# Kernel tuning notes

Hardware: AMD Instinct MI355X
Metric: run time of the kernel (lower is better)

## Reference

```python
import jax, jax.numpy as jnp
import numpy as np

N = 100000
E = 1600000
D_IN, D_HID, D_OUT = 128, 32, 32
NEG_SLOPE = 0.2
EPS = 1e-16


def setup_inputs() -> dict:
    key = jax.random.key(0)
    ks = jax.random.split(key, 9)
    x = jax.random.normal(ks[0], (N, D_IN), dtype=jnp.float32)
    edge_index = jax.random.randint(ks[1], (2, E), 0, N, dtype=jnp.int64)
    W1 = jax.random.normal(ks[2], (D_IN, D_HID), dtype=jnp.float32) / np.sqrt(D_IN)
    b1 = jnp.zeros((D_HID,), dtype=jnp.float32)
    W2 = jax.random.normal(ks[3], (D_HID, D_OUT), dtype=jnp.float32) / np.sqrt(D_HID)
    att_src = jax.random.normal(ks[4], (D_OUT,), dtype=jnp.float32) / np.sqrt(D_OUT)
    att_dst = jax.random.normal(ks[5], (D_OUT,), dtype=jnp.float32) / np.sqrt(D_OUT)
    b2 = jnp.zeros((D_OUT,), dtype=jnp.float32)
    return {"x": x, "edge_index": edge_index, "W1": W1, "b1": b1,
            "W2": W2, "att_src": att_src, "att_dst": att_dst, "b2": b2}


def _add_self_loops(edge_index, n):
    loop = jnp.arange(n, dtype=edge_index.dtype)
    src = jnp.concatenate([edge_index[0], loop])
    dst = jnp.concatenate([edge_index[1], loop])
    return src, dst


def _gcn_conv(x, src, dst, W, b, n):
    # symmetric normalization with self-loops already included
    deg = jax.ops.segment_sum(jnp.ones_like(dst, dtype=x.dtype), dst, num_segments=n)
    dis = jnp.where(deg > 0, jax.lax.rsqrt(jnp.maximum(deg, 1.0)), 0.0)
    h = x @ W                               # [N, H]
    norm = dis[src] * dis[dst]              # [E2]
    msg = norm[:, None] * h[src]            # [E2, H]
    return jax.ops.segment_sum(msg, dst, num_segments=n) + b


def _gat_conv(x, src, dst, W, att_src, att_dst, b, n):
    g = x @ W                               # [N, H]
    a_s = g @ att_src                       # [N]
    a_d = g @ att_dst                       # [N]
    e = a_s[src] + a_d[dst]                 # [E2]
    e = jnp.where(e > 0, e, NEG_SLOPE * e)  # leaky_relu(0.2)
    # segment softmax over edges grouped by destination node
    emax = jax.ops.segment_max(e, dst, num_segments=n)
    ee = jnp.exp(e - emax[dst])
    esum = jax.ops.segment_sum(ee, dst, num_segments=n)
    alpha = ee / (esum[dst] + EPS)
    msg = alpha[:, None] * g[src]           # [E2, H]
    return jax.ops.segment_sum(msg, dst, num_segments=n) + b


def reference(x, edge_index, W1, b1, W2, att_src, att_dst, b2):
    n = x.shape[0]
    src, dst = _add_self_loops(edge_index, n)
    h = _gcn_conv(x, src, dst, W1, b1, n)
    h = jax.nn.relu(h)
    out = _gat_conv(h, src, dst, W2, att_src, att_dst, b2, n)
    return out
```

## Files before the change

kernel.cpp:

```cpp
#include <hip/hip_runtime.h>
#include <cstdint>
#include <cstddef>

#define D_IN   128
#define D_HID  32
#define D_OUT  32
#define NEG_SLOPE 0.2f
#define EPS_F  1e-16f

#define BKT_SHIFT 9
#define NPB (1 << BKT_SHIFT)
#define KBUKMAX 256
#define NBLK_BIN 512
#define AGG_BLOCKS 2048

using half4 = __attribute__((ext_vector_type(4))) _Float16;

__device__ __forceinline__ int edge_val(const int* __restrict__ ei, long long idx, int is64) {
    return is64 ? ei[idx * 2] : ei[idx];
}

__device__ __forceinline__ int detect_is64(const int* __restrict__ ei, long long E,
                                           int t, int* s_is64) {
    if (t < 64) {
        long long n = E < 64 ? E : 64;
        int bad = (t < n && ei[2 * t + 1] != 0) ? 1 : 0;
        unsigned long long mask = __ballot(bad);
        if (t == 0) *s_is64 = (mask == 0ULL) ? 1 : 0;
    }
    __syncthreads();
    return *s_is64;
}

__global__ __launch_bounds__(256) void hist_kernel(
        const int* __restrict__ ei, long long E, long long E2,
        int* __restrict__ hist, int K2, int EPB) {
    __shared__ int hcnt[KBUKMAX];
    __shared__ int s_is64;
    const int t = threadIdx.x;
    if (t < K2) hcnt[t] = 0;
    const int is64 = detect_is64(ei, E, t, &s_is64);
    const long long lo = (long long)blockIdx.x * EPB;
    const long long hi = min(E2, lo + EPB);
    for (long long e = lo + t; e < hi; e += 256) {
        int d = (e < E) ? edge_val(ei, E + e, is64) : (int)(e - E);
        atomicAdd(&hcnt[d >> BKT_SHIFT], 1);
    }
    __syncthreads();
    if (t < K2) hist[t * gridDim.x + blockIdx.x] = hcnt[t];
}

__global__ void scan_ga_kernel(int* __restrict__ a, int* __restrict__ bsum, int L) {
    __shared__ int wsum[4];
    const int t = threadIdx.x;
    const int i0 = blockIdx.x * 1024 + t * 4;
    int v[4]; int s = 0;
    #pragma unroll
    for (int k = 0; k < 4; ++k) {
        v[k] = (i0 + k < L) ? a[i0 + k] : 0;
        s += v[k];
    }
    const int lane = t & 63, wid = t >> 6;
    int incl = s;
    #pragma unroll
    for (int d = 1; d < 64; d <<= 1) {
        int u = __shfl_up(incl, d);
        if (lane >= d) incl += u;
    }
    if (lane == 63) wsum[wid] = incl;
    __syncthreads();
    int woff = 0;
    for (int w = 0; w < wid; ++w) woff += wsum[w];
    int excl = woff + incl - s;
    #pragma unroll
    for (int k = 0; k < 4; ++k) {
        if (i0 + k < L) a[i0 + k] = excl;
        excl += v[k];
    }
    if (t == 255) bsum[blockIdx.x] = woff + incl;
}

__global__ __launch_bounds__(1024) void scan_flat_kernel(int* __restrict__ a, int L) {
    __shared__ int wsum[16];
    __shared__ int carry_s;
    const int t = threadIdx.x;
    const int lane = t & 63, wid = t >> 6;
    if (t == 0) carry_s = 0;
    __syncthreads();
    for (int start = 0; start < L; start += 1024) {
        int idx = start + t;
        int v = (idx < L) ? a[idx] : 0;
        int incl = v;
        #pragma unroll
        for (int d = 1; d < 64; d <<= 1) {
            int u = __shfl_up(incl, d);
            if (lane >= d) incl += u;
        }
        if (lane == 63) wsum[wid] = incl;
        __syncthreads();
        int woff = 0;
        for (int w = 0; w < wid; ++w) woff += wsum[w];
        int carry = carry_s;
        __syncthreads();
        if (idx < L) a[idx] = carry + woff + incl - v;
        if (t == 1023) carry_s = carry + woff + incl;
        __syncthreads();
    }
}

__global__ __launch_bounds__(256) void scatter_kernel(
        const int* __restrict__ ei, long long E, long long E2,
        const int* __restrict__ off, const int* __restrict__ bsum,
        unsigned* __restrict__ bins, int K2, int EPB) {
    __shared__ int cur[KBUKMAX];
    __shared__ int s_is64;
    const int t = threadIdx.x;
    if (t < K2) {
        int idx = t * gridDim.x + blockIdx.x;
        cur[t] = off[idx] + bsum[idx >> 10];
    }
    const int is64 = detect_is64(ei, E, t, &s_is64);
    const long long lo = (long long)blockIdx.x * EPB;
    const long long hi = min(E2, lo + EPB);
    for (long long e = lo + t; e < hi; e += 256) {
        int s, d;
        if (e < E) { s = edge_val(ei, e, is64); d = edge_val(ei, E + e, is64); }
        else       { s = d = (int)(e - E); }
        int b = d >> BKT_SHIFT;
        int pos = atomicAdd(&cur[b], 1);
        bins[pos] = (unsigned)s | ((unsigned)(d & (NPB - 1)) << 17);
    }
}

__global__ __launch_bounds__(512) void csr_b_kernel(
        const unsigned* __restrict__ bins, const int* __restrict__ off,
        const int* __restrict__ bsum,
        int* __restrict__ rowptr, float* __restrict__ dis, int* __restrict__ csr_src,
        int N, int K2, long long E2) {
    __shared__ int lcur[NPB];
    __shared__ int wsum[8];
    const int b = blockIdx.x, t = threadIdx.x;
    const int nbase = b << BKT_SHIFT;
    const int nn = min(NPB, N - nbase);
    lcur[t] = 0;
    __syncthreads();
    int bidx = b * NBLK_BIN;
    const int base = off[bidx] + bsum[bidx >> 10];
    int end;
    if (b == K2 - 1) end = (int)E2;
    else {
        int eidx = (b + 1) * NBLK_BIN;
        end = off[eidx] + bsum[eidx >> 10];
    }
    for (int i = base + t; i < end; i += 512)
        atomicAdd(&lcur[bins[i] >> 17], 1);
    __syncthreads();
    const int lane = t & 63, wid = t >> 6;
    int v = lcur[t];
    int incl = v;
    #pragma unroll
    for (int d = 1; d < 64; d <<= 1) {
        int u = __shfl_up(incl, d);
        if (lane >= d) incl += u;
    }
    if (lane == 63) wsum[wid] = incl;
    __syncthreads();
    int woff = 0;
    for (int w = 0; w < wid; ++w) woff += wsum[w];
    int excl = woff + incl - v;
    if (t < nn) {
        rowptr[nbase + t] = base + excl;
        dis[nbase + t] = rsqrtf((float)v);
    }
    __syncthreads();
    lcur[t] = base + excl;
    __syncthreads();
    for (int i = base + t; i < end; i += 512) {
        unsigned u = bins[i];
        int pos = atomicAdd(&lcur[u >> 17], 1);
        csr_src[pos] = (int)(u & 0x1FFFFu);
    }
    if (b == 0 && t == 0) rowptr[N] = (int)E2;
}

__global__ __launch_bounds__(256) void gemm1_kernel(
        const float* __restrict__ x, const float* __restrict__ W1,
        const float* __restrict__ dis, _Float16* __restrict__ hws_h, int N) {
    __shared__ float sW[D_IN * D_HID];
    const int t = threadIdx.x;
    for (int i = t; i < D_IN * D_HID; i += 256) sW[i] = W1[i];
    __syncthreads();
    long long row = (long long)blockIdx.x * 256 + t;
    const bool valid = row < N;
    long long r = valid ? row : (long long)(N - 1);
    const float4* x4 = (const float4*)x;
    float acc[D_HID];
    #pragma unroll
    for (int c = 0; c < D_HID; ++c) acc[c] = 0.f;
    for (int q = 0; q < 32; ++q) {
        float4 xv = x4[r * 32 + q];
        #pragma unroll
        for (int kk = 0; kk < 4; ++kk) {
            float xs = (&xv.x)[kk];
            const float* wrow = &sW[(q * 4 + kk) * D_HID];
            #pragma unroll
            for (int c4 = 0; c4 < 8; ++c4) {
                float4 wv = *(const float4*)&wrow[c4 * 4];
                acc[c4 * 4 + 0] = fmaf(xs, wv.x, acc[c4 * 4 + 0]);
                acc[c4 * 4 + 1] = fmaf(xs, wv.y, acc[c4 * 4 + 1]);
                acc[c4 * 4 + 2] = fmaf(xs, wv.z, acc[c4 * 4 + 2]);
                acc[c4 * 4 + 3] = fmaf(xs, wv.w, acc[c4 * 4 + 3]);
            }
        }
    }
    if (valid) {
        float dd = dis[r];
        half4* hh4 = (half4*)hws_h;
        #pragma unroll
        for (int c4 = 0; c4 < 8; ++c4) {
            half4 o;
            o.x = (_Float16)(acc[c4 * 4 + 0] * dd);
            o.y = (_Float16)(acc[c4 * 4 + 1] * dd);
            o.z = (_Float16)(acc[c4 * 4 + 2] * dd);
            o.w = (_Float16)(acc[c4 * 4 + 3] * dd);
            hh4[r * 8 + c4] = o;
        }
    }
}

__global__ void gcn_agg_kernel(const int* __restrict__ rowptr, const int* __restrict__ csr_src,
                               const _Float16* __restrict__ hws_h, const float* __restrict__ dis,
                               const float* __restrict__ b1, float* __restrict__ h1, int N) {
    const int lane = threadIdx.x & 63;
    const int half = lane >> 5, l32 = lane & 31;
    const int u = l32 & 7, grp = l32 >> 3;
    const int wib = threadIdx.x >> 6;
    const half4* hh4 = (const half4*)hws_h;
    float4* h14 = (float4*)h1;
    const float4 b14 = ((const float4*)b1)[u];
    const int npair = (N + 1) >> 1;
    for (int p = blockIdx.x * 4 + wib; p < npair; p += gridDim.x * 4) {
        const int i = p * 2 + half;
        const bool act = i < N;
        int b = 0, e = 0;
        if (act) { b = rowptr[i]; e = rowptr[i + 1]; }
        float ax = 0.f, ay = 0.f, az = 0.f, aw = 0.f;
        for (int j = b + grp; j < e; j += 4) {
            int s = csr_src[j];
            half4 hv = hh4[s * 8 + u];
            ax += (float)hv.x; ay += (float)hv.y;
            az += (float)hv.z; aw += (float)hv.w;
        }
        #pragma unroll
        for (int d = 8; d <= 16; d <<= 1) {
            ax += __shfl_xor(ax, d); ay += __shfl_xor(ay, d);
            az += __shfl_xor(az, d); aw += __shfl_xor(aw, d);
        }
        if (act && grp == 0) {
            float dd = dis[i];
            float4 o;
            o.x = fmaf(dd, ax, b14.x); o.y = fmaf(dd, ay, b14.y);
            o.z = fmaf(dd, az, b14.z); o.w = fmaf(dd, aw, b14.w);
            o.x = o.x > 0.f ? o.x : 0.f; o.y = o.y > 0.f ? o.y : 0.f;
            o.z = o.z > 0.f ? o.z : 0.f; o.w = o.w > 0.f ? o.w : 0.f;
            h14[(long long)i * 8 + u] = o;
        }
    }
}

__global__ void gemm2_kernel(const float* __restrict__ h1, const float* __restrict__ W2,
                             const float* __restrict__ att_s, const float* __restrict__ att_d,
                             _Float16* __restrict__ g_h, float* __restrict__ a_s,
                             float* __restrict__ a_d, int N) {
    __shared__ float sW[D_HID * D_OUT];
    __shared__ float sas[D_OUT], sad[D_OUT];
    __shared__ float sh[8][D_HID];
    const int t = threadIdx.x;
    const int c = t & 31, r = t >> 5;
    for (int i = t; i < D_HID * D_OUT; i += 256) sW[i] = W2[i];
    if (t < D_OUT) { sas[t] = att_s[t]; sad[t] = att_d[t]; }
    for (long long base = (long long)blockIdx.x * 8; base < N; base += (long long)gridDim.x * 8) {
        __syncthreads();
        if (base * D_HID + t < (long long)N * D_HID) sh[r][c] = h1[base * D_HID + t];
        __syncthreads();
        long long row = base + r;
        if (row < N) {
            float gv = 0.0f;
            #pragma unroll
            for (int k = 0; k < D_HID; ++k) gv = fmaf(sh[r][k], sW[k * D_OUT + c], gv);
            g_h[row * D_OUT + c] = (_Float16)gv;
            float ps = gv * sas[c];
            float pd = gv * sad[c];
            #pragma unroll
            for (int d = 16; d >= 1; d >>= 1) {
                ps += __shfl_xor(ps, d);
                pd += __shfl_xor(pd, d);
            }
            if (c == 0) { a_s[row] = ps; a_d[row] = pd; }
        }
    }
}

__global__ __launch_bounds__(256) void e_pre_kernel(
        const int* __restrict__ rowptr, const int* __restrict__ csr_src,
        const float* __restrict__ a_s, const float* __restrict__ a_d,
        float* __restrict__ epre, float* __restrict__ mrow, int N) {
    int i = blockIdx.x * blockDim.x + threadIdx.x;
    if (i >= N) return;
    const int b = rowptr[i], e = rowptr[i + 1];
    const float adi = a_d[i];
    float m = -1e30f;
    for (int j = b; j < e; ++j) {
        float ev = a_s[csr_src[j]] + adi;
        ev = ev > 0.f ? ev : NEG_SLOPE * ev;
        epre[j] = ev;
        m = fmaxf(m, ev);
    }
    mrow[i] = m;
}

__global__ void gat_agg_kernel(const int* __restrict__ rowptr, const int* __restrict__ csr_src,
                               const _Float16* __restrict__ g_h, const float* __restrict__ epre,
                               const float* __restrict__ mrow, const float* __restrict__ b2,
                               float* __restrict__ out, int N) {
    const int lane = threadIdx.x & 63;
    const int half = lane >> 5, l32 = lane & 31;
    const int u = l32 & 7, grp = l32 >> 3;
    const int wib = threadIdx.x >> 6;
    const half4* gh4 = (const half4*)g_h;
    float4* out4 = (float4*)out;
    const float4 b24 = ((const float4*)b2)[u];
    const int npair = (N + 1) >> 1;
    for (int p = blockIdx.x * 4 + wib; p < npair; p += gridDim.x * 4) {
        const int i = p * 2 + half;
        const bool act = i < N;
        int b = 0, e = 0;
        float mi = 0.f;
        if (act) { b = rowptr[i]; e = rowptr[i + 1]; mi = mrow[i]; }
        float ssum = 0.f;
        float ax = 0.f, ay = 0.f, az = 0.f, aw = 0.f;
        for (int j = b + grp; j < e; j += 4) {
            int s = csr_src[j];
            float w = __expf(epre[j] - mi);
            half4 gv = gh4[s * 8 + u];
            ssum += w;
            ax = fmaf(w, (float)gv.x, ax);
            ay = fmaf(w, (float)gv.y, ay);
            az = fmaf(w, (float)gv.z, az);
            aw = fmaf(w, (float)gv.w, aw);
        }
        #pragma unroll
        for (int d = 8; d <= 16; d <<= 1) {
            ssum += __shfl_xor(ssum, d);
            ax += __shfl_xor(ax, d); ay += __shfl_xor(ay, d);
            az += __shfl_xor(az, d); aw += __shfl_xor(aw, d);
        }
        if (act && grp == 0) {
            float inv = 1.f / (ssum + EPS_F);
            float4 o;
            o.x = fmaf(ax, inv, b24.x); o.y = fmaf(ay, inv, b24.y);
            o.z = fmaf(az, inv, b24.z); o.w = fmaf(aw, inv, b24.w);
            out4[(long long)i * 8 + u] = o;
        }
    }
}

extern "C" void kernel_launch(void* const* d_in, const int* in_sizes, int n_in,
                              void* d_out, int out_size, void* d_ws, size_t ws_size,
                              hipStream_t stream) {
    const float* x       = (const float*)d_in[0];
    const int*   ei      = (const int*)d_in[1];
    const float* W1      = (const float*)d_in[2];
    const float* b1      = (const float*)d_in[3];
    const float* W2      = (const float*)d_in[4];
    const float* att_src = (const float*)d_in[5];
    const float* att_dst = (const float*)d_in[6];
    const float* b2      = (const float*)d_in[7];
    float* out = (float*)d_out;

    const long long N  = in_sizes[0] / D_IN;
    const long long E  = in_sizes[1] / 2;
    const long long E2 = E + N;
    const int K2  = (int)((N + NPB - 1) >> BKT_SHIFT);
    const int EPB = (int)((E2 + NBLK_BIN - 1) / NBLK_BIN);
    const int LH  = K2 * NBLK_BIN;
    const int NBH = (LH + 1023) / 1024;

    char* ws = (char*)d_ws;
    size_t off0 = 0;
    auto alloc = [&](size_t bytes) -> void* {
        off0 = (off0 + 255) & ~(size_t)255;
        void* p = ws + off0;
        off0 += bytes;
        return p;
    };
    int*   hist     = (int*)  alloc((size_t)KBUKMAX * NBLK_BIN * 4);
    unsigned* bins  = (unsigned*)alloc((size_t)E2 * 4);
    int*   rowptr   = (int*)  alloc((size_t)(N + 1) * 4);
    int*   csr_src  = (int*)  alloc((size_t)E2 * 4);
    float* dis      = (float*)alloc((size_t)N * 4);
    _Float16* hws_h = (_Float16*)alloc((size_t)N * D_HID * 2);
    float* h1       = (float*)alloc((size_t)N * D_HID * 4);
    _Float16* g_h   = (_Float16*)alloc((size_t)N * D_OUT * 2);
    float* as       = (float*)alloc((size_t)N * 4);
    float* ad       = (float*)alloc((size_t)N * 4);
    float* epre     = (float*)alloc((size_t)E2 * 4);
    float* mrow     = (float*)alloc((size_t)N * 4);
    int*   bsum     = (int*)  alloc((size_t)NBH * 4);
    (void)ws_size; (void)n_in; (void)out_size;

    hist_kernel<<<NBLK_BIN, 256, 0, stream>>>(ei, E, E2, hist, K2, EPB);
    scan_ga_kernel<<<NBH, 256, 0, stream>>>(hist, bsum, LH);
    scan_flat_kernel<<<1, 1024, 0, stream>>>(bsum, NBH);
    scatter_kernel<<<NBLK_BIN, 256, 0, stream>>>(ei, E, E2, hist, bsum, bins, K2, EPB);
    csr_b_kernel<<<K2, 512, 0, stream>>>(bins, hist, bsum, rowptr, dis, csr_src, (int)N, K2, E2);
    gemm1_kernel<<<(int)((N + 255) / 256), 256, 0, stream>>>(x, W1, dis, hws_h, (int)N);
    gcn_agg_kernel<<<AGG_BLOCKS, 256, 0, stream>>>(rowptr, csr_src, hws_h, dis, b1, h1, (int)N);
    gemm2_kernel<<<1024, 256, 0, stream>>>(h1, W2, att_src, att_dst, g_h, as, ad, (int)N);
    e_pre_kernel<<<(int)((N + 255) / 256), 256, 0, stream>>>(rowptr, csr_src, as, ad, epre, mrow, (int)N);
    gat_agg_kernel<<<AGG_BLOCKS, 256, 0, stream>>>(rowptr, csr_src, g_h, epre, mrow, b2, out, (int)N);
}
```

Measured before the change: 180.8 us.

## Fuse GCN aggregation with second GEMM and unroll gather loops by four

Merges the GCN aggregation kernel with the W2 projection and attention-score computation. Each aggregated row is broadcast via wave shuffles and multiplied against W2 held in shared memory, which removes the fp32 h1 buffer write/read and one kernel launch. Both aggregation loops (GCN and GAT) now issue four independent gathers per iteration, raising memory-level parallelism at the cost of more registers and predicated redundant loads on short rows.

```diff
diff --git a/kernel.cpp b/kernel.cpp
--- a/kernel.cpp
+++ b/kernel.cpp
@@ -228,16 +228,26 @@
     }
 }
 
-__global__ void gcn_agg_kernel(const int* __restrict__ rowptr, const int* __restrict__ csr_src,
-                               const _Float16* __restrict__ hws_h, const float* __restrict__ dis,
-                               const float* __restrict__ b1, float* __restrict__ h1, int N) {
-    const int lane = threadIdx.x & 63;
+__global__ __launch_bounds__(256) void gcn_fused_kernel(
+        const int* __restrict__ rowptr, const int* __restrict__ csr_src,
+        const _Float16* __restrict__ hws_h, const float* __restrict__ dis,
+        const float* __restrict__ b1, const float* __restrict__ W2,
+        const float* __restrict__ att_s, const float* __restrict__ att_d,
+        _Float16* __restrict__ g_h, float* __restrict__ a_s, float* __restrict__ a_d,
+        int N) {
+    __shared__ float sW2[D_HID * D_OUT];
+    __shared__ float sas[D_OUT], sad[D_OUT];
+    const int t = threadIdx.x;
+    for (int i = t; i < D_HID * D_OUT; i += 256) sW2[i] = W2[i];
+    if (t < D_OUT) { sas[t] = att_s[t]; sad[t] = att_d[t]; }
+    __syncthreads();
+    const int lane = t & 63;
     const int half = lane >> 5, l32 = lane & 31;
     const int u = l32 & 7, grp = l32 >> 3;
-    const int wib = threadIdx.x >> 6;
+    const int wib = t >> 6;
     const half4* hh4 = (const half4*)hws_h;
-    float4* h14 = (float4*)h1;
     const float4 b14 = ((const float4*)b1)[u];
+    const int srcBase = half * 32;
     const int npair = (N + 1) >> 1;
     for (int p = blockIdx.x * 4 + wib; p < npair; p += gridDim.x * 4) {
         const int i = p * 2 + half;
@@ -245,59 +255,56 @@
         int b = 0, e = 0;
         if (act) { b = rowptr[i]; e = rowptr[i + 1]; }
         float ax = 0.f, ay = 0.f, az = 0.f, aw = 0.f;
-        for (int j = b + grp; j < e; j += 4) {
-            int s = csr_src[j];
-            half4 hv = hh4[s * 8 + u];
-            ax += (float)hv.x; ay += (float)hv.y;
-            az += (float)hv.z; aw += (float)hv.w;
+        for (int j = b + grp; j < e; j += 16) {
+            int j1 = j + 4, j2 = j + 8, j3 = j + 12;
+            bool v1 = j1 < e, v2 = j2 < e, v3 = j3 < e;
+            int s0 = csr_src[j];
+            int s1 = csr_src[v1 ? j1 : j];
+            int s2 = csr_src[v2 ? j2 : j];
+            int s3 = csr_src[v3 ? j3 : j];
+            half4 h0 = hh4[s0 * 8 + u];
+            half4 h1 = hh4[s1 * 8 + u];
+            half4 h2 = hh4[s2 * 8 + u];
+            half4 h3 = hh4[s3 * 8 + u];
+            ax += (float)h0.x + (v1 ? (float)h1.x : 0.f) + (v2 ? (float)h2.x : 0.f) + (v3 ? (float)h3.x : 0.f);
+            ay += (float)h0.y + (v1 ? (float)h1.y : 0.f) + (v2 ? (float)h2.y : 0.f) + (v3 ? (float)h3.y : 0.f);
+            az += (float)h0.z + (v1 ? (float)h1.z : 0.f) + (v2 ? (float)h2.z : 0.f) + (v3 ? (float)h3.z : 0.f);
+            aw += (float)h0.w + (v1 ? (float)h1.w : 0.f) + (v2 ? (float)h2.w : 0.f) + (v3 ? (float)h3.w : 0.f);
         }
         #pragma unroll
         for (int d = 8; d <= 16; d <<= 1) {
             ax += __shfl_xor(ax, d); ay += __shfl_xor(ay, d);
             az += __shfl_xor(az, d); aw += __shfl_xor(aw, d);
         }
-        if (act && grp == 0) {
-            float dd = dis[i];
-            float4 o;
-            o.x = fmaf(dd, ax, b14.x); o.y = fmaf(dd, ay, b14.y);
-            o.z = fmaf(dd, az, b14.z); o.w = fmaf(dd, aw, b14.w);
-            o.x = o.x > 0.f ? o.x : 0.f; o.y = o.y > 0.f ? o.y : 0.f;
-            o.z = o.z > 0.f ? o.z : 0.f; o.w = o.w > 0.f ? o.w : 0.f;
-            h14[(long long)i * 8 + u] = o;
-        }
-    }
-}
-
-__global__ void gemm2_kernel(const float* __restrict__ h1, const float* __restrict__ W2,
-                             const float* __restrict__ att_s, const float* __restrict__ att_d,
-                             _Float16* __restrict__ g_h, float* __restrict__ a_s,
-                             float* __restrict__ a_d, int N) {
-    __shared__ float sW[D_HID * D_OUT];
-    __shared__ float sas[D_OUT], sad[D_OUT];
-    __shared__ float sh[8][D_HID];
-    const int t = threadIdx.x;
-    const int c = t & 31, r = t >> 5;
-    for (int i = t; i < D_HID * D_OUT; i += 256) sW[i] = W2[i];
-    if (t < D_OUT) { sas[t] = att_s[t]; sad[t] = att_d[t]; }
-    for (long long base = (long long)blockIdx.x * 8; base < N; base += (long long)gridDim.x * 8) {
-        __syncthreads();
-        if (base * D_HID + t < (long long)N * D_HID) sh[r][c] = h1[base * D_HID + t];
-        __syncthreads();
-        long long row = base + r;
-        if (row < N) {
-            float gv = 0.0f;
-            #pragma unroll
-            for (int k = 0; k < D_HID; ++k) gv = fmaf(sh[r][k], sW[k * D_OUT + c], gv);
-            g_h[row * D_OUT + c] = (_Float16)gv;
-            float ps = gv * sas[c];
-            float pd = gv * sad[c];
-            #pragma unroll
-            for (int d = 16; d >= 1; d >>= 1) {
-                ps += __shfl_xor(ps, d);
-                pd += __shfl_xor(pd, d);
-            }
-            if (c == 0) { a_s[row] = ps; a_d[row] = pd; }
-        }
+        float dd = act ? dis[i] : 0.f;
+        float4 o;
+        o.x = fmaf(dd, ax, b14.x); o.y = fmaf(dd, ay, b14.y);
+        o.z = fmaf(dd, az, b14.z); o.w = fmaf(dd, aw, b14.w);
+        o.x = o.x > 0.f ? o.x : 0.f; o.y = o.y > 0.f ? o.y : 0.f;
+        o.z = o.z > 0.f ? o.z : 0.f; o.w = o.w > 0.f ? o.w : 0.f;
+        float gv = 0.f;
+        #pragma unroll
+        for (int up = 0; up < 8; ++up) {
+            int sl = srcBase + up;
+            float hx = __shfl(o.x, sl);
+            float hy = __shfl(o.y, sl);
+            float hz = __shfl(o.z, sl);
+            float hw = __shfl(o.w, sl);
+            const float* wr = &sW2[(up * 4) * D_OUT + l32];
+            gv = fmaf(hx, wr[0], gv);
+            gv = fmaf(hy, wr[D_OUT], gv);
+            gv = fmaf(hz, wr[2 * D_OUT], gv);
+            gv = fmaf(hw, wr[3 * D_OUT], gv);
+        }
+        if (act) g_h[(long long)i * D_OUT + l32] = (_Float16)gv;
+        float ps = gv * sas[l32];
+        float pd = gv * sad[l32];
+        #pragma unroll
+        for (int d = 1; d <= 16; d <<= 1) {
+            ps += __shfl_xor(ps, d);
+            pd += __shfl_xor(pd, d);
+        }
+        if (act && l32 == 0) { a_s[i] = ps; a_d[i] = pd; }
     }
 }
 
@@ -339,15 +346,30 @@
         if (act) { b = rowptr[i]; e = rowptr[i + 1]; mi = mrow[i]; }
         float ssum = 0.f;
         float ax = 0.f, ay = 0.f, az = 0.f, aw = 0.f;
-        for (int j = b + grp; j < e; j += 4) {
-            int s = csr_src[j];
-            float w = __expf(epre[j] - mi);
-            half4 gv = gh4[s * 8 + u];
-            ssum += w;
-            ax = fmaf(w, (float)gv.x, ax);
-            ay = fmaf(w, (float)gv.y, ay);
-            az = fmaf(w, (float)gv.z, az);
-            aw = fmaf(w, (float)gv.w, aw);
+        for (int j = b + grp; j < e; j += 16) {
+            int j1 = j + 4, j2 = j + 8, j3 = j + 12;
+            bool v1 = j1 < e, v2 = j2 < e, v3 = j3 < e;
+            int s0 = csr_src[j];
+            int s1 = csr_src[v1 ? j1 : j];
+            int s2 = csr_src[v2 ? j2 : j];
+            int s3 = csr_src[v3 ? j3 : j];
+            float e0 = epre[j];
+            float e1 = epre[v1 ? j1 : j];
+            float e2 = epre[v2 ? j2 : j];
+            float e3 = epre[v3 ? j3 : j];
+            half4 g0 = gh4[s0 * 8 + u];
+            half4 g1 = gh4[s1 * 8 + u];
+            half4 g2 = gh4[s2 * 8 + u];
+            half4 g3 = gh4[s3 * 8 + u];
+            float w0 = __expf(e0 - mi);
+            float w1 = v1 ? __expf(e1 - mi) : 0.f;
+            float w2 = v2 ? __expf(e2 - mi) : 0.f;
+            float w3 = v3 ? __expf(e3 - mi) : 0.f;
+            ssum += w0 + w1 + w2 + w3;
+            ax = fmaf(w0, (float)g0.x, fmaf(w1, (float)g1.x, fmaf(w2, (float)g2.x, fmaf(w3, (float)g3.x, ax))));
+            ay = fmaf(w0, (float)g0.y, fmaf(w1, (float)g1.y, fmaf(w2, (float)g2.y, fmaf(w3, (float)g3.y, ay))));
+            az = fmaf(w0, (float)g0.z, fmaf(w1, (float)g1.z, fmaf(w2, (float)g2.z, fmaf(w3, (float)g3.z, az))));
+            aw = fmaf(w0, (float)g0.w, fmaf(w1, (float)g1.w, fmaf(w2, (float)g2.w, fmaf(w3, (float)g3.w, aw))));
         }
         #pragma unroll
         for (int d = 8; d <= 16; d <<= 1) {
@@ -400,7 +422,6 @@
     int*   csr_src  = (int*)  alloc((size_t)E2 * 4);
     float* dis      = (float*)alloc((size_t)N * 4);
     _Float16* hws_h = (_Float16*)alloc((size_t)N * D_HID * 2);
-    float* h1       = (float*)alloc((size_t)N * D_HID * 4);
     _Float16* g_h   = (_Float16*)alloc((size_t)N * D_OUT * 2);
     float* as       = (float*)alloc((size_t)N * 4);
     float* ad       = (float*)alloc((size_t)N * 4);
@@ -415,8 +436,8 @@
     scatter_kernel<<<NBLK_BIN, 256, 0, stream>>>(ei, E, E2, hist, bsum, bins, K2, EPB);
     csr_b_kernel<<<K2, 512, 0, stream>>>(bins, hist, bsum, rowptr, dis, csr_src, (int)N, K2, E2);
     gemm1_kernel<<<(int)((N + 255) / 256), 256, 0, stream>>>(x, W1, dis, hws_h, (int)N);
-    gcn_agg_kernel<<<AGG_BLOCKS, 256, 0, stream>>>(rowptr, csr_src, hws_h, dis, b1, h1, (int)N);
-    gemm2_kernel<<<1024, 256, 0, stream>>>(h1, W2, att_src, att_dst, g_h, as, ad, (int)N);
+    gcn_fused_kernel<<<AGG_BLOCKS, 256, 0, stream>>>(rowptr, csr_src, hws_h, dis, b1, W2,
+                                                     att_src, att_dst, g_h, as, ad, (int)N);
     e_pre_kernel<<<(int)((N + 255) / 256), 256, 0, stream>>>(rowptr, csr_src, as, ad, epre, mrow, (int)N);
     gat_agg_kernel<<<AGG_BLOCKS, 256, 0, stream>>>(rowptr, csr_src, g_h, epre, mrow, b2, out, (int)N);
 }
```

New measurement: 162.9 us. 1.11x faster.
